# Optimization experiments

Hardware: AMD Instinct MI355X
Metric: run time of the kernel (lower is better)

The kernel has to match this reference:

```python
import jax, jax.numpy as jnp
import numpy as np

H = 12        # num_attention_heads
A = 16        # agent_num
C = 768       # hidden_size


def setup_inputs() -> dict:
    key = jax.random.key(0)
    ks = jax.random.split(key, 16)
    B, N = 8, 4096
    std = 0.02
    return {
        "s1_hidden_states": jax.random.normal(ks[0], (B, N, C), jnp.float32),
        "s2_hidden_states": jax.random.normal(ks[1], (B, N, C), jnp.float32),
        "Wq": jax.random.normal(ks[2], (C, C), jnp.float32) * std,
        "bq": jnp.zeros((C,), jnp.float32),
        "Wk": jax.random.normal(ks[3], (C, C), jnp.float32) * std,
        "bk": jnp.zeros((C,), jnp.float32),
        "Wv": jax.random.normal(ks[4], (C, C), jnp.float32) * std,
        "bv": jnp.zeros((C,), jnp.float32),
        "an_bias": jax.random.normal(ks[5], (H, A, 7, 7), jnp.float32) * std,
        "na_bias": jax.random.normal(ks[6], (H, A, 7, 7), jnp.float32) * std,
        "ah_bias": jax.random.normal(ks[7], (1, H, A, A, 1), jnp.float32) * std,
        "aw_bias": jax.random.normal(ks[8], (1, H, A, 1, A), jnp.float32) * std,
        "ha_bias": jax.random.normal(ks[9], (1, H, A, 1, A), jnp.float32) * std,
        "wa_bias": jax.random.normal(ks[10], (1, H, 1, A, A), jnp.float32) * std,
    }


def reference(s1_hidden_states, s2_hidden_states, Wq, bq, Wk, bk, Wv, bv,
              an_bias, na_bias, ah_bias, aw_bias, ha_bias, wa_bias):
    b, n, c = s1_hidden_states.shape
    m = s2_hidden_states.shape[1]
    hd = c // H
    scale = hd ** -0.5

    q = s1_hidden_states @ Wq.T + bq            # (b, n, c)
    k = s2_hidden_states @ Wk.T + bk            # (b, m, c)
    v = s2_hidden_states @ Wv.T + bv            # (b, m, c)

    # AdaptiveAvgPool1d(A) with n % A == 0 -> uniform chunk mean
    agent = q.reshape(b, A, n // A, c).mean(axis=2)  # (b, A, c)

    def heads(x):
        return x.reshape(b, -1, H, hd).transpose(0, 2, 1, 3)

    qh, kh, vh = heads(q), heads(k), heads(v)        # (b,H,·,hd)
    ah = heads(agent)                                # (b,H,A,hd)

    # stage 1: agent -> keys.  bias is constant per (h, a) row.
    pb1 = jax.image.resize(an_bias, (H, A, A, A), method='bilinear').reshape(1, H, A, A * A)
    pb2 = (ah_bias + aw_bias).reshape(1, H, A, A * A)
    pb = (pb1 + pb2).mean(axis=-1)                   # (1, H, A)
    agent_attn = jnp.einsum('bhad,bhmd->bham', ah * scale, kh) + pb[:, :, :, None]
    agent_attn = jax.nn.softmax(agent_attn, axis=-1)
    agent_v = jnp.einsum('bham,bhmd->bhad', agent_attn, vh)  # (b,H,A,hd)

    # stage 2: queries -> agents.
    ab1 = jax.image.resize(na_bias, (H, A, A, A), method='bilinear') \
            .reshape(1, H, A, A * A).transpose(0, 1, 3, 2)   # (1,H,A*A,A)
    ab2 = (ha_bias + wa_bias).reshape(1, H, A * A, A)
    ab = (ab1 + ab2).mean(axis=-2)                   # (1, H, A)
    q_attn = jnp.einsum('bhnd,bhad->bhna', qh * scale, ah) + ab[:, :, None, :]
    q_attn = jax.nn.softmax(q_attn, axis=-1)
    x = jnp.einsum('bhna,bhad->bhnd', q_attn, agent_v)  # (b,H,n,hd)
    return x.transpose(0, 2, 1, 3).reshape(b, n, c)
```

## Files before the change

kernel.cpp:

```cpp
#include <hip/hip_runtime.h>
#include <cstdint>
#include <cstddef>

typedef unsigned short ushort_t;
typedef unsigned int uint;

typedef __attribute__((ext_vector_type(8))) short short8;
typedef __attribute__((ext_vector_type(4))) float floatx4;

#define CDIM 768

__device__ __forceinline__ float bfu(ushort_t u) {
    return __uint_as_float(((uint)u) << 16);
}
__device__ __forceinline__ void bf2(uint u, float& lo, float& hi) {
    lo = __uint_as_float(u << 16);
    hi = __uint_as_float(u & 0xffff0000u);
}
__device__ __forceinline__ ushort_t f2bfu(float f) {
    uint u = __float_as_uint(f);
    u += 0x7fffu + ((u >> 16) & 1u);
    return (ushort_t)(u >> 16);
}
__device__ __forceinline__ uint pack2(float a, float b) {
    return (uint)f2bfu(a) | ((uint)f2bfu(b) << 16);
}
__device__ __forceinline__ uint cvt2(float lo, float hi) {
    uint r;
    asm("v_cvt_pk_bf16_f32 %0, %1, %2" : "=v"(r) : "v"(lo), "v"(hi));
    return r;
}
__device__ __forceinline__ short8 mk8(uint a, uint b, uint c, uint d) {
    union { uint4 u; short8 s; } x;
    x.u = (uint4){a, b, c, d};
    return x.s;
}
__device__ __forceinline__ void gload_lds16(const void* g, void* l) {
    __builtin_amdgcn_global_load_lds(
        (__attribute__((address_space(1))) void*)(uintptr_t)g,
        (__attribute__((address_space(3))) void*)l, 16, 0, 0);
}

__global__ __launch_bounds__(256) void prep(
    const float* __restrict__ Wq, const float* __restrict__ Wk,
    const float* __restrict__ Wv, const float* __restrict__ bq,
    const float* __restrict__ na, const float* __restrict__ ha,
    const float* __restrict__ wa,
    ushort_t* __restrict__ wb, float* __restrict__ agent, float* __restrict__ ab)
{
    const int bid = blockIdx.x;
    if (bid < 864) {
        const int m = bid / 288;
        const float* src = (m == 0) ? Wq : (m == 1 ? Wk : Wv);
        ushort_t* dst = wb + (size_t)m * 589824;
        const int i = ((bid % 288) * 256 + threadIdx.x) * 8;
        const float4 f0 = *(const float4*)(src + i);
        const float4 f1 = *(const float4*)(src + i + 4);
        uint4 u;
        u.x = pack2(f0.x, f0.y);
        u.y = pack2(f0.z, f0.w);
        u.z = pack2(f1.x, f1.y);
        u.w = pack2(f1.z, f1.w);
        *(uint4*)(dst + i) = u;
    } else if (bid < 960) {
        const int bh = bid - 864;
        const int h = bh % 12;
        for (int i = threadIdx.x; i < 1024; i += 256)
            agent[(size_t)bh * 1024 + i] = bq[h * 64 + (i & 63)];
    } else {
        const int t = threadIdx.x;
        if (t >= 192) return;
        const int h = t >> 4, a = t & 15;
        const float cw[7] = {2.25f, 2.34375f, 2.28125f, 2.25f, 2.28125f, 2.34375f, 2.25f};
        float acc = 0.f;
        const float* nb = na + (h * 16 + a) * 49;
        for (int i = 0; i < 7; ++i)
            for (int j = 0; j < 7; ++j)
                acc += cw[i] * cw[j] * nb[i * 7 + j];
        acc *= (1.0f / 256.0f);
        float s = 0.f;
        for (int p = 0; p < 16; ++p)
            s += ha[(h * 16 + p) * 16 + a] + wa[(h * 16 + p) * 16 + a];
        ab[t] = acc + s * (1.0f / 16.0f);
    }
}

__global__ __launch_bounds__(256) void cvt_a(
    const float* __restrict__ s1, const float* __restrict__ s2,
    ushort_t* __restrict__ ab)
{
    const int m = blockIdx.y;
    const float* src = (m == 0) ? s1 : s2;
    ushort_t* dst = ab + (size_t)m * 25165824;
    const size_t i = ((size_t)blockIdx.x * 256 + threadIdx.x) * 8;
    const float4 f0 = *(const float4*)(src + i);
    const float4 f1 = *(const float4*)(src + i + 4);
    uint4 u;
    u.x = pack2(f0.x, f0.y);
    u.y = pack2(f0.z, f0.w);
    u.z = pack2(f1.x, f1.y);
    u.w = pack2(f1.z, f1.w);
    *(uint4*)(dst + i) = u;
}

__global__ __launch_bounds__(256, 2) void gemm_qkv(
    const ushort_t* __restrict__ ab, const ushort_t* __restrict__ wb,
    const float* __restrict__ bq, const float* __restrict__ bk, const float* __restrict__ bv,
    ushort_t* __restrict__ qo, ushort_t* __restrict__ ko, ushort_t* __restrict__ vo,
    float* __restrict__ agent)
{
    const int z = blockIdx.z;
    const ushort_t* A     = ab + (size_t)(z != 0) * 25165824;
    const ushort_t* W     = wb + (size_t)z * 589824;
    const float* bias     = (z == 0) ? bq : (z == 1 ? bk : bv);
    ushort_t* out         = (z == 0) ? qo : (z == 1 ? ko : vo);

    __shared__ ushort_t lds[17408];
    ushort_t* At = lds;
    ushort_t* Wt = lds + 8192;

    const int tid  = threadIdx.x;
    const int wave = tid >> 6;
    const int lane = tid & 63;
    const int wm = wave >> 1, wn = wave & 1;

    const int id   = blockIdx.x + (blockIdx.y << 8);
    const int id2  = (id & 7) * 192 + (id >> 3);
    const int row0 = (id2 / 6) * 128;
    const int col0 = (id2 % 6) * 128;

    const int sro = lane >> 3;
    const int sch = ((lane & 7) ^ sro) * 8;
    const ushort_t* gaBase = A + (size_t)(row0 + wave * 32 + sro) * CDIM + sch;
    const ushort_t* gwBase = W + (size_t)(col0 + wave * 32 + sro) * CDIM + sch;

    floatx4 acc[4][4];
    #pragma unroll
    for (int i = 0; i < 4; ++i)
        #pragma unroll
        for (int j = 0; j < 4; ++j)
            acc[i][j] = (floatx4){0.f, 0.f, 0.f, 0.f};

    const int q4 = lane >> 4, r16 = lane & 15;

    for (int kt = 0; kt < CDIM; kt += 64) {
        __syncthreads();
        #pragma unroll
        for (int i = 0; i < 4; ++i) {
            gload_lds16(gaBase + (size_t)i * 8 * CDIM + kt, &At[(wave * 32 + i * 8) * 64]);
            gload_lds16(gwBase + (size_t)i * 8 * CDIM + kt, &Wt[(wave * 32 + i * 8) * 64]);
        }
        __syncthreads();
        #pragma unroll
        for (int ks = 0; ks < 2; ++ks) {
            short8 af[4], bfr[4];
            #pragma unroll
            for (int mt = 0; mt < 4; ++mt) {
                const int row = wm * 64 + mt * 16 + r16;
                const int ch  = (ks * 4 + q4) ^ (row & 7);
                af[mt] = *(const short8*)&At[row * 64 + ch * 8];
            }
            #pragma unroll
            for (int nt = 0; nt < 4; ++nt) {
                const int row = wn * 64 + nt * 16 + r16;
                const int ch  = (ks * 4 + q4) ^ (row & 7);
                bfr[nt] = *(const short8*)&Wt[row * 64 + ch * 8];
            }
            #pragma unroll
            for (int mt = 0; mt < 4; ++mt)
                #pragma unroll
                for (int nt = 0; nt < 4; ++nt)
                    acc[mt][nt] = __builtin_amdgcn_mfma_f32_16x16x32_bf16(
                        af[mt], bfr[nt], acc[mt][nt], 0, 0, 0);
        }
    }

    __syncthreads();
    const int b = row0 >> 12;
    const int m_base = row0 & 4095;
    #pragma unroll
    for (int nt = 0; nt < 4; ++nt) {
        const int coll = wn * 64 + nt * 16 + r16;
        const float bb = bias[col0 + coll];
        float psum = 0.f;
        #pragma unroll
        for (int mt = 0; mt < 4; ++mt) {
            const int rowl = wm * 64 + mt * 16 + q4 * 4;
            #pragma unroll
            for (int r = 0; r < 4; ++r) {
                lds[(rowl + r) * 136 + coll] = f2bfu(acc[mt][nt][r] + bb);
                psum += acc[mt][nt][r];
            }
        }
        if (z == 0) {
            psum += __shfl_xor(psum, 16);
            psum += __shfl_xor(psum, 32);
            if (q4 == 0) {
                const int h = (col0 + coll) >> 6, d = (col0 + coll) & 63;
                atomicAdd(&agent[(size_t)(b * 12 + h) * 1024 + (m_base >> 8) * 64 + d],
                          psum * (1.0f / 256.0f));
            }
        }
    }
    __syncthreads();
    #pragma unroll
    for (int it = 0; it < 8; ++it) {
        const int task  = it * 256 + tid;
        const int chunk = task & 7;
        const int rh    = task >> 3;
        const int rowl  = rh >> 1, hl = rh & 1;
        const uint4 v = *(const uint4*)&lds[rowl * 136 + hl * 64 + chunk * 8];
        ushort_t* op = out + ((size_t)(b * 12 + (col0 >> 6) + hl) * 4096
                              + m_base + rowl) * 64 + chunk * 8;
        *(uint4*)op = v;
    }
}

__global__ __launch_bounds__(512) void stage1(
    const ushort_t* __restrict__ k_hm, const ushort_t* __restrict__ v_hm,
    const float* __restrict__ agent, float* __restrict__ Sp, float* __restrict__ avp)
{
    const int bh = blockIdx.x, z = blockIdx.y;
    const int tid = threadIdx.x;
    __shared__ float ahs[1024];
    __shared__ ushort_t E2[512 * 20];

    for (int i = tid; i < 1024; i += 512)
        ahs[i] = agent[(size_t)bh * 1024 + i] * 0.125f;
    __syncthreads();

    const int m0 = z * 512;
    const ushort_t* kb = k_hm + ((size_t)bh * 4096 + m0) * 64;

    {
        const uint4* kr = (const uint4*)(kb + (size_t)tid * 64);
        uint ku[32];
        #pragma unroll
        for (int i = 0; i < 8; ++i) {
            uint4 ua = kr[i];
            ku[i*4+0] = ua.x; ku[i*4+1] = ua.y; ku[i*4+2] = ua.z; ku[i*4+3] = ua.w;
        }
        float ds[16];
        #pragma unroll
        for (int a = 0; a < 16; ++a) ds[a] = 0.f;
        #pragma unroll
        for (int c = 0; c < 16; ++c) {
            float a0, a1, a2, a3;
            bf2(ku[2*c],   a0, a1); bf2(ku[2*c+1], a2, a3);
            #pragma unroll
            for (int a = 0; a < 16; ++a) {
                const floatx4 av = *(const floatx4*)&ahs[a * 64 + c * 4];
                ds[a] += a0 * av[0] + a1 * av[1] + a2 * av[2] + a3 * av[3];
            }
        }
        uint e[8];
        #pragma unroll
        for (int a2 = 0; a2 < 8; ++a2)
            e[a2] = pack2(__expf(ds[2*a2]), __expf(ds[2*a2+1]));
        uint2* dA = (uint2*)&E2[(size_t)tid * 20];
        dA[0] = make_uint2(e[0], e[1]); dA[1] = make_uint2(e[2], e[3]);
        dA[2] = make_uint2(e[4], e[5]); dA[3] = make_uint2(e[6], e[7]);
    }
    __syncthreads();

    const int d = tid & 63, g = (tid >> 6) & 3, half = tid >> 8;
    const int mb = half * 256;
    const ushort_t* vb = v_hm + ((size_t)bh * 4096 + m0 + mb) * 64 + d;
    float acc0 = 0, acc1 = 0, acc2 = 0, acc3 = 0;
    float ss0 = 0, ss1 = 0, ss2 = 0, ss3 = 0;
    for (int ml = 0; ml < 256; ++ml) {
        const float vv = bfu(vb[(size_t)ml * 64]);
        const uint2 ee = *(const uint2*)&E2[(size_t)(mb + ml) * 20 + g * 4];
        float e0, e1, e2, e3;
        bf2(ee.x, e0, e1);
        bf2(ee.y, e2, e3);
        acc0 += e0 * vv; ss0 += e0;
        acc1 += e1 * vv; ss1 += e1;
        acc2 += e2 * vv; ss2 += e2;
        acc3 += e3 * vv; ss3 += e3;
    }
    const int z2 = z * 2 + half;
    float* avz = avp + (size_t)(z2 * 96 + bh) * 1024;
    avz[(g * 4 + 0) * 64 + d] = acc0;
    avz[(g * 4 + 1) * 64 + d] = acc1;
    avz[(g * 4 + 2) * 64 + d] = acc2;
    avz[(g * 4 + 3) * 64 + d] = acc3;
    if (d == 0) {
        float* Sz = Sp + (z2 * 96 + bh) * 16;
        Sz[g * 4 + 0] = ss0;
        Sz[g * 4 + 1] = ss1;
        Sz[g * 4 + 2] = ss2;
        Sz[g * 4 + 3] = ss3;
    }
}

__global__ __launch_bounds__(256) void stage2(
    const ushort_t* __restrict__ q_hm, const float* __restrict__ avp,
    const float* __restrict__ Sp, const float* __restrict__ agent,
    const float* __restrict__ ab, float* __restrict__ out)
{
    const int nb = blockIdx.x;
    const int bh = blockIdx.y;
    const int b = bh / 12, h = bh % 12;
    const int tid = threadIdx.x;
    const int g = (tid >> 4) & 3;
    const int t = tid & 15;
    const int w = tid >> 6;
    __shared__ float avn[1024];

    {
        const int i4 = tid * 4;
        const int a = i4 >> 6;
        floatx4 num = {0.f, 0.f, 0.f, 0.f};
        float den = 0.f;
        #pragma unroll
        for (int zz = 0; zz < 16; ++zz) {
            num += *(const floatx4*)&avp[(size_t)(zz * 96 + bh) * 1024 + i4];
            den += Sp[(zz * 96 + bh) * 16 + a];
        }
        const float r = 1.0f / den;
        *(floatx4*)&avn[i4] = num * r;
    }
    __syncthreads();

    short8 ahA[2], ahE[2];
    #pragma unroll
    for (int k0 = 0; k0 < 2; ++k0) {
        const float* p = agent + (size_t)bh * 1024 + t * 64 + k0 * 32 + g * 8;
        const float4 f0 = *(const float4*)p;
        const float4 f1 = *(const float4*)(p + 4);
        const float v[8] = {f0.x, f0.y, f0.z, f0.w, f1.x, f1.y, f1.z, f1.w};
        uint u[4], e[4];
        #pragma unroll
        for (int j = 0; j < 4; ++j) {
            const float a0 = v[2*j] * 0.125f, a1 = v[2*j+1] * 0.125f;
            u[j] = cvt2(a0, a1);
            float b0, b1; bf2(u[j], b0, b1);
            e[j] = cvt2(a0 - b0, a1 - b1);
        }
        ahA[k0] = mk8(u[0], u[1], u[2], u[3]);
        ahE[k0] = mk8(e[0], e[1], e[2], e[3]);
    }

    short8 avf[4], ave[4];
    #pragma unroll
    for (int dt = 0; dt < 4; ++dt) {
        uint u[4] = {0, 0, 0, 0}, e[4] = {0, 0, 0, 0};
        if (g < 2) {
            #pragma unroll
            for (int j = 0; j < 4; ++j) {
                const float a0 = avn[(8*g + 2*j)     * 64 + dt * 16 + t];
                const float a1 = avn[(8*g + 2*j + 1) * 64 + dt * 16 + t];
                u[j] = cvt2(a0, a1);
                float b0, b1; bf2(u[j], b0, b1);
                e[j] = cvt2(a0 - b0, a1 - b1);
            }
        }
        avf[dt] = mk8(u[0], u[1], u[2], u[3]);
        ave[dt] = mk8(e[0], e[1], e[2], e[3]);
    }

    float abv[4];
    #pragma unroll
    for (int r = 0; r < 4; ++r) abv[r] = ab[h * 16 + 4 * g + r];

    const int src0 = (t + 32 * g) & 63;
    const int src1 = (src0 + 16) & 63;
    const int n0 = nb * 256 + w * 64;
    const ushort_t* qb = q_hm + ((size_t)bh * 4096 + n0) * 64;
    float* ob = out + ((size_t)b * 4096 + n0) * CDIM + h * 64;

    #pragma unroll
    for (int ti = 0; ti < 4; ++ti) {
        const ushort_t* qp = qb + (size_t)(ti * 16 + t) * 64 + g * 8;
        const short8 qB0 = *(const short8*)(qp);
        const short8 qB1 = *(const short8*)(qp + 32);

        floatx4 sc = {0.f, 0.f, 0.f, 0.f};
        sc = __builtin_amdgcn_mfma_f32_16x16x32_bf16(ahA[0], qB0, sc, 0, 0, 0);
        sc = __builtin_amdgcn_mfma_f32_16x16x32_bf16(ahA[1], qB1, sc, 0, 0, 0);
        sc = __builtin_amdgcn_mfma_f32_16x16x32_bf16(ahE[0], qB0, sc, 0, 0, 0);
        sc = __builtin_amdgcn_mfma_f32_16x16x32_bf16(ahE[1], qB1, sc, 0, 0, 0);

        const float e0 = __expf(sc[0] + abv[0]);
        const float e1 = __expf(sc[1] + abv[1]);
        const float e2 = __expf(sc[2] + abv[2]);
        const float e3 = __expf(sc[3] + abv[3]);
        float s = e0 + e1 + e2 + e3;
        s += __shfl_xor(s, 16);
        s += __shfl_xor(s, 32);
        const float rs = 1.0f / s;
        const float p0 = e0 * rs, p1 = e1 * rs, p2 = e2 * rs, p3 = e3 * rs;

        const uint P0 = cvt2(p0, p1), P1 = cvt2(p2, p3);
        float q0, q1, q2, q3;
        bf2(P0, q0, q1); bf2(P1, q2, q3);
        const uint E0 = cvt2(p0 - q0, p1 - q1), E1 = cvt2(p2 - q2, p3 - q3);

        uint w0 = __shfl(P0, src0), w1 = __shfl(P1, src0);
        uint w2 = __shfl(P0, src1), w3 = __shfl(P1, src1);
        uint x0 = __shfl(E0, src0), x1 = __shfl(E1, src0);
        uint x2 = __shfl(E0, src1), x3 = __shfl(E1, src1);
        if (g >= 2) { w0 = w1 = w2 = w3 = 0; x0 = x1 = x2 = x3 = 0; }
        const short8 pf = mk8(w0, w1, w2, w3);
        const short8 pe = mk8(x0, x1, x2, x3);

        float* op = ob + (size_t)(ti * 16 + t) * CDIM + 4 * g;
        #pragma unroll
        for (int dt = 0; dt < 4; ++dt) {
            floatx4 od = {0.f, 0.f, 0.f, 0.f};
            od = __builtin_amdgcn_mfma_f32_16x16x32_bf16(avf[dt], pf, od, 0, 0, 0);
            od = __builtin_amdgcn_mfma_f32_16x16x32_bf16(avf[dt], pe, od, 0, 0, 0);
            od = __builtin_amdgcn_mfma_f32_16x16x32_bf16(ave[dt], pf, od, 0, 0, 0);
            *(floatx4*)(op + dt * 16) = od;
        }
    }
}

extern "C" void kernel_launch(void* const* d_in, const int* in_sizes, int n_in,
                              void* d_out, int out_size, void* d_ws, size_t ws_size,
                              hipStream_t stream) {
    (void)in_sizes; (void)n_in; (void)out_size; (void)ws_size;
    const float* s1 = (const float*)d_in[0];
    const float* s2 = (const float*)d_in[1];
    const float* Wq = (const float*)d_in[2];
    const float* bq = (const float*)d_in[3];
    const float* Wk = (const float*)d_in[4];
    const float* bk = (const float*)d_in[5];
    const float* Wv = (const float*)d_in[6];
    const float* bv = (const float*)d_in[7];
    const float* na = (const float*)d_in[9];
    const float* ha = (const float*)d_in[12];
    const float* wa = (const float*)d_in[13];
    float* out = (float*)d_out;

    char* ws = (char*)d_ws;
    ushort_t* q_hm = (ushort_t*)(ws);
    ushort_t* k_hm = (ushort_t*)(ws + 50331648);
    ushort_t* v_hm = (ushort_t*)(ws + 100663296);
    float* agent   = (float*)(ws + 150994944);
    float* Sp      = (float*)(ws + 151388160);
    float* ab      = (float*)(ws + 151486464);
    ushort_t* wb   = (ushort_t*)(ws + 151487232);
    ushort_t* abuf = (ushort_t*)(ws + 155026176);
    float* avp     = (float*)(ws + 155026176);

    prep     <<<dim3(961),       256, 0, stream>>>(Wq, Wk, Wv, bq, na, ha, wa,
                                                   wb, agent, ab);
    cvt_a    <<<dim3(12288, 2),  256, 0, stream>>>(s1, s2, abuf);
    gemm_qkv <<<dim3(256, 6, 3), 256, 0, stream>>>(abuf, wb, bq, bk, bv,
                                                   q_hm, k_hm, v_hm, agent);
    stage1   <<<dim3(96, 8),     512, 0, stream>>>(k_hm, v_hm, agent, Sp, avp);
    stage2   <<<dim3(16, 96),    256, 0, stream>>>(q_hm, avp, Sp, agent, ab, out);
}
```

Baseline: 295.8 us.

## Compute stage1 agent-key scores with bf16 MFMA and double the key split

Result: faster. 278.3 us (-5.9%).

```diff
diff --git a/kernel.cpp b/kernel.cpp
--- a/kernel.cpp
+++ b/kernel.cpp
@@ -222,55 +222,59 @@
 {
     const int bh = blockIdx.x, z = blockIdx.y;
     const int tid = threadIdx.x;
-    __shared__ float ahs[1024];
-    __shared__ ushort_t E2[512 * 20];
-
-    for (int i = tid; i < 1024; i += 512)
-        ahs[i] = agent[(size_t)bh * 1024 + i] * 0.125f;
+    const int lane = tid & 63;
+    const int w = tid >> 6;
+    const int g = lane >> 4;
+    const int t = lane & 15;
+    __shared__ ushort_t E2[256 * 20];
+
+    short8 ahA[2], ahE[2];
+    #pragma unroll
+    for (int k0 = 0; k0 < 2; ++k0) {
+        const float* p = agent + (size_t)bh * 1024 + t * 64 + k0 * 32 + g * 8;
+        const float4 f0 = *(const float4*)p;
+        const float4 f1 = *(const float4*)(p + 4);
+        const float v[8] = {f0.x, f0.y, f0.z, f0.w, f1.x, f1.y, f1.z, f1.w};
+        uint u[4], e[4];
+        #pragma unroll
+        for (int j = 0; j < 4; ++j) {
+            const float a0 = v[2*j] * 0.125f, a1 = v[2*j+1] * 0.125f;
+            u[j] = cvt2(a0, a1);
+            float b0, b1; bf2(u[j], b0, b1);
+            e[j] = cvt2(a0 - b0, a1 - b1);
+        }
+        ahA[k0] = mk8(u[0], u[1], u[2], u[3]);
+        ahE[k0] = mk8(e[0], e[1], e[2], e[3]);
+    }
+
+    const int m0 = z * 256;
+    const ushort_t* kb = k_hm + ((size_t)bh * 4096 + m0) * 64;
+
+    #pragma unroll
+    for (int ti = 0; ti < 2; ++ti) {
+        const int row = w * 32 + ti * 16 + t;
+        const ushort_t* kp = kb + (size_t)row * 64 + g * 8;
+        const short8 kB0 = *(const short8*)(kp);
+        const short8 kB1 = *(const short8*)(kp + 32);
+        floatx4 sc = {0.f, 0.f, 0.f, 0.f};
+        sc = __builtin_amdgcn_mfma_f32_16x16x32_bf16(ahA[0], kB0, sc, 0, 0, 0);
+        sc = __builtin_amdgcn_mfma_f32_16x16x32_bf16(ahA[1], kB1, sc, 0, 0, 0);
+        sc = __builtin_amdgcn_mfma_f32_16x16x32_bf16(ahE[0], kB0, sc, 0, 0, 0);
+        sc = __builtin_amdgcn_mfma_f32_16x16x32_bf16(ahE[1], kB1, sc, 0, 0, 0);
+        const uint P0 = pack2(__expf(sc[0]), __expf(sc[1]));
+        const uint P1 = pack2(__expf(sc[2]), __expf(sc[3]));
+        *(uint2*)&E2[(size_t)row * 20 + g * 4] = make_uint2(P0, P1);
+    }
     __syncthreads();
 
-    const int m0 = z * 512;
-    const ushort_t* kb = k_hm + ((size_t)bh * 4096 + m0) * 64;
-
-    {
-        const uint4* kr = (const uint4*)(kb + (size_t)tid * 64);
-        uint ku[32];
-        #pragma unroll
-        for (int i = 0; i < 8; ++i) {
-            uint4 ua = kr[i];
-            ku[i*4+0] = ua.x; ku[i*4+1] = ua.y; ku[i*4+2] = ua.z; ku[i*4+3] = ua.w;
-        }
-        float ds[16];
-        #pragma unroll
-        for (int a = 0; a < 16; ++a) ds[a] = 0.f;
-        #pragma unroll
-        for (int c = 0; c < 16; ++c) {
-            float a0, a1, a2, a3;
-            bf2(ku[2*c],   a0, a1); bf2(ku[2*c+1], a2, a3);
-            #pragma unroll
-            for (int a = 0; a < 16; ++a) {
-                const floatx4 av = *(const floatx4*)&ahs[a * 64 + c * 4];
-                ds[a] += a0 * av[0] + a1 * av[1] + a2 * av[2] + a3 * av[3];
-            }
-        }
-        uint e[8];
-        #pragma unroll
-        for (int a2 = 0; a2 < 8; ++a2)
-            e[a2] = pack2(__expf(ds[2*a2]), __expf(ds[2*a2+1]));
-        uint2* dA = (uint2*)&E2[(size_t)tid * 20];
-        dA[0] = make_uint2(e[0], e[1]); dA[1] = make_uint2(e[2], e[3]);
-        dA[2] = make_uint2(e[4], e[5]); dA[3] = make_uint2(e[6], e[7]);
-    }
-    __syncthreads();
-
-    const int d = tid & 63, g = (tid >> 6) & 3, half = tid >> 8;
-    const int mb = half * 256;
+    const int d = tid & 63, gg = (tid >> 6) & 3, half = tid >> 8;
+    const int mb = half * 128;
     const ushort_t* vb = v_hm + ((size_t)bh * 4096 + m0 + mb) * 64 + d;
     float acc0 = 0, acc1 = 0, acc2 = 0, acc3 = 0;
     float ss0 = 0, ss1 = 0, ss2 = 0, ss3 = 0;
-    for (int ml = 0; ml < 256; ++ml) {
+    for (int ml = 0; ml < 128; ++ml) {
         const float vv = bfu(vb[(size_t)ml * 64]);
-        const uint2 ee = *(const uint2*)&E2[(size_t)(mb + ml) * 20 + g * 4];
+        const uint2 ee = *(const uint2*)&E2[(size_t)(mb + ml) * 20 + gg * 4];
         float e0, e1, e2, e3;
         bf2(ee.x, e0, e1);
         bf2(ee.y, e2, e3);
@@ -281,16 +285,16 @@
     }
     const int z2 = z * 2 + half;
     float* avz = avp + (size_t)(z2 * 96 + bh) * 1024;
-    avz[(g * 4 + 0) * 64 + d] = acc0;
-    avz[(g * 4 + 1) * 64 + d] = acc1;
-    avz[(g * 4 + 2) * 64 + d] = acc2;
-    avz[(g * 4 + 3) * 64 + d] = acc3;
+    avz[(gg * 4 + 0) * 64 + d] = acc0;
+    avz[(gg * 4 + 1) * 64 + d] = acc1;
+    avz[(gg * 4 + 2) * 64 + d] = acc2;
+    avz[(gg * 4 + 3) * 64 + d] = acc3;
     if (d == 0) {
         float* Sz = Sp + (z2 * 96 + bh) * 16;
-        Sz[g * 4 + 0] = ss0;
-        Sz[g * 4 + 1] = ss1;
-        Sz[g * 4 + 2] = ss2;
-        Sz[g * 4 + 3] = ss3;
+        Sz[gg * 4 + 0] = ss0;
+        Sz[gg * 4 + 1] = ss1;
+        Sz[gg * 4 + 2] = ss2;
+        Sz[gg * 4 + 3] = ss3;
     }
 }
 
@@ -314,7 +318,7 @@
         floatx4 num = {0.f, 0.f, 0.f, 0.f};
         float den = 0.f;
         #pragma unroll
-        for (int zz = 0; zz < 16; ++zz) {
+        for (int zz = 0; zz < 32; ++zz) {
             num += *(const floatx4*)&avp[(size_t)(zz * 96 + bh) * 1024 + i4];
             den += Sp[(zz * 96 + bh) * 16 + a];
         }
@@ -440,16 +444,16 @@
     ushort_t* v_hm = (ushort_t*)(ws + 100663296);
     float* agent   = (float*)(ws + 150994944);
     float* Sp      = (float*)(ws + 151388160);
-    float* ab      = (float*)(ws + 151486464);
-    ushort_t* wb   = (ushort_t*)(ws + 151487232);
-    ushort_t* abuf = (ushort_t*)(ws + 155026176);
-    float* avp     = (float*)(ws + 155026176);
+    float* ab      = (float*)(ws + 151584768);
+    ushort_t* wb   = (ushort_t*)(ws + 151585536);
+    ushort_t* abuf = (ushort_t*)(ws + 155124480);
+    float* avp     = (float*)(ws + 155124480);
 
     prep     <<<dim3(961),       256, 0, stream>>>(Wq, Wk, Wv, bq, na, ha, wa,
                                                    wb, agent, ab);
     cvt_a    <<<dim3(12288, 2),  256, 0, stream>>>(s1, s2, abuf);
     gemm_qkv <<<dim3(256, 6, 3), 256, 0, stream>>>(abuf, wb, bq, bk, bv,
                                                    q_hm, k_hm, v_hm, agent);
-    stage1   <<<dim3(96, 8),     512, 0, stream>>>(k_hm, v_hm, agent, Sp, avp);
+    stage1   <<<dim3(96, 16),    512, 0, stream>>>(k_hm, v_hm, agent, Sp, avp);
     stage2   <<<dim3(16, 96),    256, 0, stream>>>(q_hm, avp, Sp, agent, ab, out);
 }
```
